# Kernel tuning notes

Measured on AMD Instinct MI355X. Metric: run time of the kernel, lower is better.

## Reference

```python
import jax, jax.numpy as jnp
import numpy as np

BN, SN = 16, 64
C, T, FY, FX = 480, 8, 28, 28
OS = 8            # roialign output_size
NDF = 256
K = 64            # n_clusters
ALPHA = 1.0
IMG_W, IMG_H = 1920.0, 1080.0
SPATIAL_SCALE = 1.0


def _roi_align(feat, boxes):
    """torchvision RoIAlign with sampling_ratio=1, aligned=True.
    feat: [bn, C, H, W]; boxes: [bn, sn, 4] (x1,y1,x2,y2) in feature coords.
    Returns [bn, sn, C, OS, OS]."""
    bn, c, H, W = feat.shape
    xy1 = boxes[..., 0:2] * SPATIAL_SCALE - 0.5   # aligned=True offset
    xy2 = boxes[..., 2:4] * SPATIAL_SCALE - 0.5
    bin_wh = (xy2 - xy1) / OS                     # [bn,sn,2]
    ctr = jnp.arange(OS, dtype=feat.dtype) + 0.5  # one sample per bin (ratio=1)
    xs = xy1[..., 0:1] + ctr * bin_wh[..., 0:1]   # [bn,sn,OS]
    ys = xy1[..., 1:2] + ctr * bin_wh[..., 1:2]
    X = xs[:, :, None, :]                         # [bn,sn,1,OS]
    Y = ys[:, :, :, None]                         # [bn,sn,OS,1]
    valid = (Y > -1.0) & (Y < H) & (X > -1.0) & (X < W)
    x = jnp.clip(X, 0.0, W - 1.0)
    y = jnp.clip(Y, 0.0, H - 1.0)
    x0 = jnp.floor(x).astype(jnp.int32)
    y0 = jnp.floor(y).astype(jnp.int32)
    x1 = jnp.minimum(x0 + 1, W - 1)
    y1 = jnp.minimum(y0 + 1, H - 1)
    lx = x - x0
    ly = y - y0
    fhw = jnp.transpose(feat, (0, 2, 3, 1))       # [bn,H,W,C]
    g = jax.vmap(lambda f, yy, xx: f[yy, xx])     # broadcasting gather -> [bn,sn,OS,OS,C]
    v00 = g(fhw, y0, x0); v01 = g(fhw, y0, x1)
    v10 = g(fhw, y1, x0); v11 = g(fhw, y1, x1)
    wy0, wy1 = (1.0 - ly)[..., None], ly[..., None]
    wx0, wx1 = (1.0 - lx)[..., None], lx[..., None]
    out = v00 * wy0 * wx0 + v01 * wy0 * wx1 + v10 * wy1 * wx0 + v11 * wy1 * wx1
    out = jnp.where(valid[..., None], out, 0.0)
    return jnp.transpose(out, (0, 1, 4, 2, 3))    # [bn,sn,C,OS,OS] (torch layout)


def setup_inputs() -> dict:
    key = jax.random.key(0)
    ks = jax.random.split(key, 6)
    z_vis = jax.random.normal(ks[0], (BN, C, T, FY, FX), jnp.float32)
    # valid boxes (x1<x2, y1<y2), fully inside the image -> no NaN padding rows
    tl = jax.random.uniform(ks[1], (BN, SN, 2)) * jnp.array([IMG_W * 0.5, IMG_H * 0.5])
    wh = jax.random.uniform(ks[2], (BN, SN, 2)) * jnp.array([IMG_W * 0.4, IMG_H * 0.4]) + 16.0
    bboxs = jnp.concatenate([tl, tl + wh], axis=-1).astype(jnp.float32)
    W_vis = jax.random.normal(ks[3], (C * OS * OS, NDF), jnp.float32) / np.sqrt(C * OS * OS)
    b_vis = jnp.zeros((NDF,), jnp.float32)
    W_spc = jax.random.normal(ks[4], (1, NDF), jnp.float32)
    b_spc = jnp.zeros((NDF,), jnp.float32)
    centroids = jax.random.normal(ks[5], (K, NDF), jnp.float32) * 0.1
    return {"z_vis": z_vis, "bboxs": bboxs, "W_vis": W_vis, "b_vis": b_vis,
            "W_spc": W_spc, "b_spc": b_spc, "centroids": centroids}


def reference(z_vis, bboxs, W_vis, b_vis, W_spc, b_spc, centroids):
    bn, sn = bboxs.shape[:2]
    # scale image-coord boxes to feature-map coords
    scale = jnp.array([FX / IMG_W, FY / IMG_H], dtype=z_vis.dtype)
    boxes_f = (bboxs.reshape(bn, sn, 2, 2) * scale).reshape(bn, sn, 4)
    feat = z_vis[:, :, -1]                                   # last temporal frame [bn,C,fy,fx]
    roi = _roi_align(feat, boxes_f).reshape(bn, sn, -1)      # [bn,sn,C*OS*OS]
    z_v = roi @ W_vis + b_vis                                # visual embedding [bn,sn,NDF]
    # spatial embedding: normalized distance of bbox center to image center (detached)
    b2 = bboxs.reshape(bn, sn, 2, 2)
    ctr = b2[:, :, 0] + (b2[:, :, 1] - b2[:, :, 0]) * 0.5    # [bn,sn,2]
    img_c = jnp.array([IMG_W / 2.0, IMG_H / 2.0], dtype=z_vis.dtype)
    norms = jnp.linalg.norm(ctr - img_c, axis=-1, keepdims=True) / jnp.linalg.norm(img_c)
    norms = jax.lax.stop_gradient(norms)                     # .detach() in original
    z_s = norms @ W_spc + b_spc                              # [bn,sn,NDF]
    z = z_v + z_s
    # Student-t soft assignment on L2 distance (NOT squared, as in the source)
    d = jnp.linalg.norm(z[:, :, None, :] - centroids, axis=-1)   # [bn,sn,K]
    s_un = (1.0 + d / ALPHA) ** (-(ALPHA + 1.0) / 2.0)
    s = s_un / jnp.sum(s_un, axis=-1, keepdims=True)
    c = jnp.argmax(s, axis=-1)
    return z, s, c
```

## Files before the change

kernel.cpp:

```cpp
#include <hip/hip_runtime.h>
#include <cstdint>
#include <cstddef>

#define BN_   16
#define C_    480
#define T_    8
#define FY_   28
#define FX_   28
#define NDF_  256
#define KC_   64
#define M_    1024
#define KD_   30720
#define PLANE_ 784
#define CHSTRIDE_ (T_*PLANE_)
#define CT_   (C_*CHSTRIDE_)
#define KS_   32
#define KCH_  960
#define NCH_  15
#define NSTEP_ 30
#define MT_   32
#define APAD_ 72
#define BTILE_ 16384

typedef __attribute__((ext_vector_type(8))) short bf16x8;
typedef __attribute__((ext_vector_type(4))) float f32x4;

__device__ __forceinline__ unsigned rne_bf16(float f) {
    union { float f; unsigned u; } v; v.f = f;
    return v.u + 0x7FFFu + ((v.u >> 16) & 1u);
}
__device__ __forceinline__ float bfbits_to_f(unsigned r) {
    union { unsigned u; float f; } v; v.u = r & 0xFFFF0000u;
    return v.f;
}

__global__ __launch_bounds__(256)
void convert_pack(const float* __restrict__ W, unsigned short* __restrict__ Bpack) {
    const int blk = blockIdx.x;
    const int kb = blk * 32;
    const int n = threadIdx.x;
    unsigned hw[16], lw[16];
    #pragma unroll
    for (int p = 0; p < 16; ++p) {
        const float v0 = W[(size_t)(kb + 2 * p) * NDF_ + n];
        const float v1 = W[(size_t)(kb + 2 * p + 1) * NDF_ + n];
        const unsigned h0 = rne_bf16(v0), h1 = rne_bf16(v1);
        const unsigned l0 = rne_bf16(v0 - bfbits_to_f(h0));
        const unsigned l1 = rne_bf16(v1 - bfbits_to_f(h1));
        hw[p] = __builtin_amdgcn_perm(h1, h0, 0x07060302u);
        lw[p] = __builtin_amdgcn_perm(l1, l0, 0x07060302u);
    }
    unsigned short* hb = Bpack + (size_t)blk * BTILE_;
    unsigned short* lb = hb + 8192;
    uint4* ho = (uint4*)hb + n * 4;
    uint4* lo = (uint4*)lb + n * 4;
    #pragma unroll
    for (int q = 0; q < 4; ++q) {
        ho[q] = make_uint4(hw[q * 4 + 0], hw[q * 4 + 1], hw[q * 4 + 2], hw[q * 4 + 3]);
        lo[q] = make_uint4(lw[q * 4 + 0], lw[q * 4 + 1], lw[q * 4 + 2], lw[q * 4 + 3]);
    }
}

__global__ void convert_cent(const float* __restrict__ cent, float* __restrict__ centT) {
    const int k = blockIdx.x;
    const int j = threadIdx.x;
    centT[(size_t)j * KC_ + k] = cent[(size_t)k * NDF_ + j];
}

__global__ __launch_bounds__(256, 3)
void gemm_fused(const float* __restrict__ z_vis, const unsigned short* __restrict__ Bpack,
                const float* __restrict__ bboxs, float* __restrict__ z_acc) {
    __shared__ short Ah[MT_ * APAD_];
    __shared__ short Al[MT_ * APAD_];
    __shared__ unsigned short Bh[256 * 32];
    __shared__ unsigned short Bl[256 * 32];
    __shared__ float Pl[PLANE_];

    const int t = threadIdx.x;
    const int ks = blockIdx.x, mi = blockIdx.y;
    const int lane = t & 63, wid = t >> 6;

    const int m = t >> 3, by = t & 7;
    const int roi = mi * MT_ + m;
    const int bn = mi >> 1;

    int xi0[8], xi1[8];
    float xw0[8], xw1[8];
    int yr0, yr1;
    float wy0v, wy1v;
    {
        const float bx1 = bboxs[roi * 4 + 0], by1 = bboxs[roi * 4 + 1];
        const float bx2 = bboxs[roi * 4 + 2], by2 = bboxs[roi * 4 + 3];
        const float sx = 28.0f / 1920.0f, sy = 28.0f / 1080.0f;
        const float lo_x = bx1 * sx - 0.5f;
        const float binw_x = (bx2 * sx - 0.5f - lo_x) * 0.125f;
        const float lo_y = by1 * sy - 0.5f;
        const float binw_y = (by2 * sy - 0.5f - lo_y) * 0.125f;
        #pragma unroll
        for (int b = 0; b < 8; ++b) {
            const float pos = lo_x + ((float)b + 0.5f) * binw_x;
            const float vx = (pos > -1.0f && pos < 28.0f) ? 1.0f : 0.0f;
            const float pc = fminf(fmaxf(pos, 0.0f), 27.0f);
            const float p0 = floorf(pc);
            const float lx = pc - p0;
            xi0[b] = (int)p0;
            xi1[b] = min(xi0[b] + 1, 27);
            xw0[b] = vx * (1.0f - lx);
            xw1[b] = vx * lx;
        }
        const float pos = lo_y + ((float)by + 0.5f) * binw_y;
        const float vy = (pos > -1.0f && pos < 28.0f) ? 1.0f : 0.0f;
        const float pc = fminf(fmaxf(pos, 0.0f), 27.0f);
        const float p0 = floorf(pc);
        const float ly = pc - p0;
        const int y0 = (int)p0, y1 = min(y0 + 1, 27);
        yr0 = y0 * FX_; yr1 = y1 * FX_;
        wy0v = vy * (1.0f - ly); wy1v = vy * ly;
    }
    const float* plane = z_vis + (size_t)bn * CT_ + (size_t)(T_ - 1) * PLANE_;

    auto plane_load = [&](int cc) {
        if (wid != 0) return;
        const char* gb = (const char*)(plane + (size_t)(ks * NCH_ + cc) * CHSTRIDE_);
        #pragma unroll
        for (int i = 0; i < 3; ++i)
            __builtin_amdgcn_global_load_lds(
                (const __attribute__((address_space(1))) void*)(gb + (i * 64 + lane) * 16),
                (__attribute__((address_space(3))) void*)((char*)Pl + i * 1024), 16, 0, 0);
        if (lane < 4)
            __builtin_amdgcn_global_load_lds(
                (const __attribute__((address_space(1))) void*)(gb + (192 + lane) * 16),
                (__attribute__((address_space(3))) void*)((char*)Pl + 3072), 16, 0, 0);
    };

    auto stage_B = [&](int s) {
        const unsigned short* hb = Bpack + (size_t)(ks * NSTEP_ + s) * BTILE_;
        #pragma unroll
        for (int qq = 0; qq < 4; ++qq) {
            const int off = (qq * 64 + wid * 16) * 32;
            __builtin_amdgcn_global_load_lds(
                (const __attribute__((address_space(1))) void*)(hb + off + lane * 8),
                (__attribute__((address_space(3))) void*)&Bh[off], 16, 0, 0);
            __builtin_amdgcn_global_load_lds(
                (const __attribute__((address_space(1))) void*)(hb + 8192 + off + lane * 8),
                (__attribute__((address_space(3))) void*)&Bl[off], 16, 0, 0);
        }
    };

    auto stage_A = [&]() {
        unsigned rh[8], rl[8];
        #pragma unroll
        for (int b = 0; b < 8; ++b) {
            const float v00 = Pl[yr0 + xi0[b]], v01 = Pl[yr0 + xi1[b]];
            const float v10 = Pl[yr1 + xi0[b]], v11 = Pl[yr1 + xi1[b]];
            const float val = wy0v * (xw0[b] * v00 + xw1[b] * v01)
                            + wy1v * (xw0[b] * v10 + xw1[b] * v11);
            rh[b] = rne_bf16(val);
            rl[b] = rne_bf16(val - bfbits_to_f(rh[b]));
        }
        const uint4 hh = make_uint4(__builtin_amdgcn_perm(rh[1], rh[0], 0x07060302u),
                                    __builtin_amdgcn_perm(rh[3], rh[2], 0x07060302u),
                                    __builtin_amdgcn_perm(rh[5], rh[4], 0x07060302u),
                                    __builtin_amdgcn_perm(rh[7], rh[6], 0x07060302u));
        const uint4 ll = make_uint4(__builtin_amdgcn_perm(rl[1], rl[0], 0x07060302u),
                                    __builtin_amdgcn_perm(rl[3], rl[2], 0x07060302u),
                                    __builtin_amdgcn_perm(rl[5], rl[4], 0x07060302u),
                                    __builtin_amdgcn_perm(rl[7], rl[6], 0x07060302u));
        *(uint4*)&Ah[m * APAD_ + by * 8] = hh;
        *(uint4*)&Al[m * APAD_ + by * 8] = ll;
    };

    const int fr = lane & 15, fq = lane >> 4;
    f32x4 acc[2][4] = {};

    plane_load(0);
    stage_B(0);
    __syncthreads();
    stage_A();

    for (int cc = 0; cc < NCH_; ++cc) {
        #pragma unroll
        for (int half = 0; half < 2; ++half) {
            const int s = 2 * cc + half;
            __syncthreads();

            bf16x8 afh[2], afl[2], bh[4], bl[4];
            #pragma unroll
            for (int i = 0; i < 2; ++i) {
                afh[i] = *(const bf16x8*)&Ah[(i * 16 + fr) * APAD_ + half * 32 + fq * 8];
                afl[i] = *(const bf16x8*)&Al[(i * 16 + fr) * APAD_ + half * 32 + fq * 8];
            }
            #pragma unroll
            for (int j = 0; j < 4; ++j) {
                bh[j] = *(const bf16x8*)&Bh[(wid * 64 + j * 16 + fr) * 32 + fq * 8];
                bl[j] = *(const bf16x8*)&Bl[(wid * 64 + j * 16 + fr) * 32 + fq * 8];
            }
            __syncthreads();

            if (half == 0) {
                stage_B(s + 1);
                if (cc + 1 < NCH_) plane_load(cc + 1);
            } else if (cc + 1 < NCH_) {
                stage_B(s + 1);
                stage_A();
            }

            #pragma unroll
            for (int j = 0; j < 4; ++j)
                #pragma unroll
                for (int i = 0; i < 2; ++i) {
                    acc[i][j] = __builtin_amdgcn_mfma_f32_16x16x32_bf16(afh[i], bh[j], acc[i][j], 0, 0, 0);
                    acc[i][j] = __builtin_amdgcn_mfma_f32_16x16x32_bf16(afl[i], bh[j], acc[i][j], 0, 0, 0);
                    acc[i][j] = __builtin_amdgcn_mfma_f32_16x16x32_bf16(afh[i], bl[j], acc[i][j], 0, 0, 0);
                }
        }
    }

    #pragma unroll
    for (int i = 0; i < 2; ++i) {
        const int row = mi * MT_ + i * 16 + fq * 4;
        #pragma unroll
        for (int j = 0; j < 4; ++j) {
            const int col = wid * 64 + j * 16 + fr;
            #pragma unroll
            for (int r = 0; r < 4; ++r)
                atomicAdd(&z_acc[(size_t)(row + r) * NDF_ + col], acc[i][j][r]);
        }
    }
}

__global__ __launch_bounds__(256)
void cluster_kernel(const float* __restrict__ z_acc, const float* __restrict__ bboxs,
                    const float* __restrict__ b_vis, const float* __restrict__ W_spc,
                    const float* __restrict__ b_spc, const float* __restrict__ centT,
                    float* __restrict__ out) {
    const int row = blockIdx.x, t = threadIdx.x;
    __shared__ float zs[NDF_];
    __shared__ float dp[4][KC_];

    const float a = z_acc[(size_t)row * NDF_ + t];

    const float x1 = bboxs[row * 4 + 0], y1 = bboxs[row * 4 + 1];
    const float x2 = bboxs[row * 4 + 2], y2 = bboxs[row * 4 + 3];
    const float cx = x1 + (x2 - x1) * 0.5f - 960.0f;
    const float cy = y1 + (y2 - y1) * 0.5f - 540.0f;
    const float nrm = sqrtf(cx * cx + cy * cy) / sqrtf(960.0f * 960.0f + 540.0f * 540.0f);

    const float zj = a + b_vis[t] + nrm * W_spc[t] + b_spc[t];
    zs[t] = zj;
    out[(size_t)row * NDF_ + t] = zj;
    __syncthreads();

    const int k = t & 63, qq = t >> 6;
    {
        float d2 = 0.0f;
        const float* ct = centT + (size_t)qq * 64 * KC_;
        #pragma unroll 8
        for (int j = 0; j < 64; ++j) {
            const float df = zs[qq * 64 + j] - ct[(size_t)j * KC_ + k];
            d2 += df * df;
        }
        dp[qq][k] = d2;
    }
    __syncthreads();

    if (t < 64) {
        const float d = sqrtf(dp[0][t] + dp[1][t] + dp[2][t] + dp[3][t]);
        const float su = 1.0f / (1.0f + d);
        float sum = su;
        #pragma unroll
        for (int mk = 1; mk < 64; mk <<= 1) sum += __shfl_xor(sum, mk, 64);
        out[(size_t)M_ * NDF_ + (size_t)row * KC_ + t] = su / sum;
        float v = d; int idx = t;
        #pragma unroll
        for (int mk = 1; mk < 64; mk <<= 1) {
            const float ov = __shfl_xor(v, mk, 64);
            const int oi = __shfl_xor(idx, mk, 64);
            if (ov < v || (ov == v && oi < idx)) { v = ov; idx = oi; }
        }
        if (t == 0)
            out[(size_t)M_ * NDF_ + (size_t)M_ * KC_ + row] = (float)idx;
    }
}

extern "C" void kernel_launch(void* const* d_in, const int* in_sizes, int n_in,
                              void* d_out, int out_size, void* d_ws, size_t ws_size,
                              hipStream_t stream) {
    const float* z_vis = (const float*)d_in[0];
    const float* bboxs = (const float*)d_in[1];
    const float* W_vis = (const float*)d_in[2];
    const float* b_vis = (const float*)d_in[3];
    const float* W_spc = (const float*)d_in[4];
    const float* b_spc = (const float*)d_in[5];
    const float* cent  = (const float*)d_in[6];
    float* out = (float*)d_out;

    char* ws = (char*)d_ws;
    unsigned short* Bpack = (unsigned short*)ws;
    float*          centT = (float*)(ws + 31457280);
    float*          z_acc = (float*)(ws + 31457280 + 65536);

    convert_pack<<<KS_ * NSTEP_, 256, 0, stream>>>(W_vis, Bpack);
    convert_cent<<<KC_, 256, 0, stream>>>(cent, centT);
    hipMemsetAsync(z_acc, 0, (size_t)M_ * NDF_ * sizeof(float), stream);
    gemm_fused<<<dim3(KS_, M_ / MT_), 256, 0, stream>>>(z_vis, Bpack, bboxs, z_acc);
    cluster_kernel<<<M_, 256, 0, stream>>>(z_acc, bboxs, b_vis, W_spc, b_spc, centT, out);
}
```

Before: 370.4 us.

## Double M tile to one batch per block and restage LDS layouts conflict-free

Result: faster. 346.9 us (-6.3%).

```diff
diff --git a/kernel.cpp b/kernel.cpp
--- a/kernel.cpp
+++ b/kernel.cpp
@@ -18,8 +18,8 @@
 #define KCH_  960
 #define NCH_  15
 #define NSTEP_ 30
-#define MT_   32
-#define APAD_ 72
+#define MT_   64
+#define AOS_  520
 #define BTILE_ 16384
 
 typedef __attribute__((ext_vector_type(8))) short bf16x8;
@@ -32,6 +32,10 @@
 __device__ __forceinline__ float bfbits_to_f(unsigned r) {
     union { unsigned u; float f; } v; v.u = r & 0xFFFF0000u;
     return v.f;
+}
+__device__ __forceinline__ void lds_dma16(const void* g, void* l) {
+    __builtin_amdgcn_global_load_lds((const __attribute__((address_space(1))) void*)g,
+                                     (__attribute__((address_space(3))) void*)l, 16, 0, 0);
 }
 
 __global__ __launch_bounds__(256)
@@ -50,14 +54,12 @@
         hw[p] = __builtin_amdgcn_perm(h1, h0, 0x07060302u);
         lw[p] = __builtin_amdgcn_perm(l1, l0, 0x07060302u);
     }
-    unsigned short* hb = Bpack + (size_t)blk * BTILE_;
-    unsigned short* lb = hb + 8192;
-    uint4* ho = (uint4*)hb + n * 4;
-    uint4* lo = (uint4*)lb + n * 4;
+    uint4* hb4 = (uint4*)(Bpack + (size_t)blk * BTILE_);
+    uint4* lb4 = hb4 + 1024;
     #pragma unroll
-    for (int q = 0; q < 4; ++q) {
-        ho[q] = make_uint4(hw[q * 4 + 0], hw[q * 4 + 1], hw[q * 4 + 2], hw[q * 4 + 3]);
-        lo[q] = make_uint4(lw[q * 4 + 0], lw[q * 4 + 1], lw[q * 4 + 2], lw[q * 4 + 3]);
+    for (int o = 0; o < 4; ++o) {
+        hb4[o * 256 + n] = make_uint4(hw[o * 4 + 0], hw[o * 4 + 1], hw[o * 4 + 2], hw[o * 4 + 3]);
+        lb4[o * 256 + n] = make_uint4(lw[o * 4 + 0], lw[o * 4 + 1], lw[o * 4 + 2], lw[o * 4 + 3]);
     }
 }
 
@@ -67,27 +69,26 @@
     centT[(size_t)j * KC_ + k] = cent[(size_t)k * NDF_ + j];
 }
 
-__global__ __launch_bounds__(256, 3)
+__global__ __launch_bounds__(256, 2)
 void gemm_fused(const float* __restrict__ z_vis, const unsigned short* __restrict__ Bpack,
                 const float* __restrict__ bboxs, float* __restrict__ z_acc) {
-    __shared__ short Ah[MT_ * APAD_];
-    __shared__ short Al[MT_ * APAD_];
-    __shared__ unsigned short Bh[256 * 32];
-    __shared__ unsigned short Bl[256 * 32];
+    __shared__ short Ah[8 * AOS_];
+    __shared__ short Al[8 * AOS_];
+    __shared__ unsigned short Bh[8192];
+    __shared__ unsigned short Bl[8192];
     __shared__ float Pl[PLANE_];
 
     const int t = threadIdx.x;
     const int ks = blockIdx.x, mi = blockIdx.y;
     const int lane = t & 63, wid = t >> 6;
 
-    const int m = t >> 3, by = t & 7;
+    const int m = t >> 2, byl = t & 3;
     const int roi = mi * MT_ + m;
-    const int bn = mi >> 1;
 
     int xi0[8], xi1[8];
     float xw0[8], xw1[8];
-    int yr0, yr1;
-    float wy0v, wy1v;
+    int yr0[2], yr1[2];
+    float wy0[2], wy1[2];
     {
         const float bx1 = bboxs[roi * 4 + 0], by1 = bboxs[roi * 4 + 1];
         const float bx2 = bboxs[roi * 4 + 2], by2 = bboxs[roi * 4 + 3];
@@ -108,70 +109,71 @@
             xw0[b] = vx * (1.0f - lx);
             xw1[b] = vx * lx;
         }
-        const float pos = lo_y + ((float)by + 0.5f) * binw_y;
-        const float vy = (pos > -1.0f && pos < 28.0f) ? 1.0f : 0.0f;
-        const float pc = fminf(fmaxf(pos, 0.0f), 27.0f);
-        const float p0 = floorf(pc);
-        const float ly = pc - p0;
-        const int y0 = (int)p0, y1 = min(y0 + 1, 27);
-        yr0 = y0 * FX_; yr1 = y1 * FX_;
-        wy0v = vy * (1.0f - ly); wy1v = vy * ly;
-    }
-    const float* plane = z_vis + (size_t)bn * CT_ + (size_t)(T_ - 1) * PLANE_;
+        #pragma unroll
+        for (int h = 0; h < 2; ++h) {
+            const int by = byl + h * 4;
+            const float pos = lo_y + ((float)by + 0.5f) * binw_y;
+            const float vy = (pos > -1.0f && pos < 28.0f) ? 1.0f : 0.0f;
+            const float pc = fminf(fmaxf(pos, 0.0f), 27.0f);
+            const float p0 = floorf(pc);
+            const float ly = pc - p0;
+            const int y0 = (int)p0, y1 = min(y0 + 1, 27);
+            yr0[h] = y0 * FX_; yr1[h] = y1 * FX_;
+            wy0[h] = vy * (1.0f - ly); wy1[h] = vy * ly;
+        }
+    }
+    const float* plane = z_vis + (size_t)mi * CT_ + (size_t)(T_ - 1) * PLANE_;
 
     auto plane_load = [&](int cc) {
-        if (wid != 0) return;
         const char* gb = (const char*)(plane + (size_t)(ks * NCH_ + cc) * CHSTRIDE_);
-        #pragma unroll
-        for (int i = 0; i < 3; ++i)
-            __builtin_amdgcn_global_load_lds(
-                (const __attribute__((address_space(1))) void*)(gb + (i * 64 + lane) * 16),
-                (__attribute__((address_space(3))) void*)((char*)Pl + i * 1024), 16, 0, 0);
-        if (lane < 4)
-            __builtin_amdgcn_global_load_lds(
-                (const __attribute__((address_space(1))) void*)(gb + (192 + lane) * 16),
-                (__attribute__((address_space(3))) void*)((char*)Pl + 3072), 16, 0, 0);
+        if (wid < 3) {
+            lds_dma16(gb + (wid * 64 + lane) * 16, (char*)Pl + wid * 1024);
+        } else if (lane < 4) {
+            lds_dma16(gb + (192 + lane) * 16, (char*)Pl + 3072);
+        }
     };
 
     auto stage_B = [&](int s) {
-        const unsigned short* hb = Bpack + (size_t)(ks * NSTEP_ + s) * BTILE_;
+        const char* hb = (const char*)(Bpack + (size_t)(ks * NSTEP_ + s) * BTILE_);
         #pragma unroll
         for (int qq = 0; qq < 4; ++qq) {
-            const int off = (qq * 64 + wid * 16) * 32;
-            __builtin_amdgcn_global_load_lds(
-                (const __attribute__((address_space(1))) void*)(hb + off + lane * 8),
-                (__attribute__((address_space(3))) void*)&Bh[off], 16, 0, 0);
-            __builtin_amdgcn_global_load_lds(
-                (const __attribute__((address_space(1))) void*)(hb + 8192 + off + lane * 8),
-                (__attribute__((address_space(3))) void*)&Bl[off], 16, 0, 0);
+            const int chunk = (qq * 4 + wid) * 1024;
+            lds_dma16(hb + chunk + lane * 16, (char*)Bh + chunk);
+            lds_dma16(hb + 16384 + chunk + lane * 16, (char*)Bl + chunk);
         }
     };
 
     auto stage_A = [&]() {
-        unsigned rh[8], rl[8];
-        #pragma unroll
-        for (int b = 0; b < 8; ++b) {
-            const float v00 = Pl[yr0 + xi0[b]], v01 = Pl[yr0 + xi1[b]];
-            const float v10 = Pl[yr1 + xi0[b]], v11 = Pl[yr1 + xi1[b]];
-            const float val = wy0v * (xw0[b] * v00 + xw1[b] * v01)
-                            + wy1v * (xw0[b] * v10 + xw1[b] * v11);
-            rh[b] = rne_bf16(val);
-            rl[b] = rne_bf16(val - bfbits_to_f(rh[b]));
-        }
-        const uint4 hh = make_uint4(__builtin_amdgcn_perm(rh[1], rh[0], 0x07060302u),
-                                    __builtin_amdgcn_perm(rh[3], rh[2], 0x07060302u),
-                                    __builtin_amdgcn_perm(rh[5], rh[4], 0x07060302u),
-                                    __builtin_amdgcn_perm(rh[7], rh[6], 0x07060302u));
-        const uint4 ll = make_uint4(__builtin_amdgcn_perm(rl[1], rl[0], 0x07060302u),
-                                    __builtin_amdgcn_perm(rl[3], rl[2], 0x07060302u),
-                                    __builtin_amdgcn_perm(rl[5], rl[4], 0x07060302u),
-                                    __builtin_amdgcn_perm(rl[7], rl[6], 0x07060302u));
-        *(uint4*)&Ah[m * APAD_ + by * 8] = hh;
-        *(uint4*)&Al[m * APAD_ + by * 8] = ll;
+        #pragma unroll
+        for (int h = 0; h < 2; ++h) {
+            const int by = byl + h * 4;
+            const int r0 = yr0[h], r1 = yr1[h];
+            const float w0 = wy0[h], w1 = wy1[h];
+            unsigned rh[8], rl[8];
+            #pragma unroll
+            for (int b = 0; b < 8; ++b) {
+                const float v00 = Pl[r0 + xi0[b]], v01 = Pl[r0 + xi1[b]];
+                const float v10 = Pl[r1 + xi0[b]], v11 = Pl[r1 + xi1[b]];
+                const float val = w0 * (xw0[b] * v00 + xw1[b] * v01)
+                                + w1 * (xw0[b] * v10 + xw1[b] * v11);
+                rh[b] = rne_bf16(val);
+                rl[b] = rne_bf16(val - bfbits_to_f(rh[b]));
+            }
+            const uint4 hh = make_uint4(__builtin_amdgcn_perm(rh[1], rh[0], 0x07060302u),
+                                        __builtin_amdgcn_perm(rh[3], rh[2], 0x07060302u),
+                                        __builtin_amdgcn_perm(rh[5], rh[4], 0x07060302u),
+                                        __builtin_amdgcn_perm(rh[7], rh[6], 0x07060302u));
+            const uint4 ll = make_uint4(__builtin_amdgcn_perm(rl[1], rl[0], 0x07060302u),
+                                        __builtin_amdgcn_perm(rl[3], rl[2], 0x07060302u),
+                                        __builtin_amdgcn_perm(rl[5], rl[4], 0x07060302u),
+                                        __builtin_amdgcn_perm(rl[7], rl[6], 0x07060302u));
+            *(uint4*)&Ah[by * AOS_ + m * 8] = hh;
+            *(uint4*)&Al[by * AOS_ + m * 8] = ll;
+        }
     };
 
     const int fr = lane & 15, fq = lane >> 4;
-    f32x4 acc[2][4] = {};
+    f32x4 acc[4][4] = {};
 
     plane_load(0);
     stage_B(0);
@@ -184,16 +186,18 @@
             const int s = 2 * cc + half;
             __syncthreads();
 
-            bf16x8 afh[2], afl[2], bh[4], bl[4];
-            #pragma unroll
-            for (int i = 0; i < 2; ++i) {
-                afh[i] = *(const bf16x8*)&Ah[(i * 16 + fr) * APAD_ + half * 32 + fq * 8];
-                afl[i] = *(const bf16x8*)&Al[(i * 16 + fr) * APAD_ + half * 32 + fq * 8];
+            bf16x8 afh[4], afl[4], bh[4], bl[4];
+            #pragma unroll
+            for (int i = 0; i < 4; ++i) {
+                const int ao = (half * 4 + fq) * AOS_ + (i * 16 + fr) * 8;
+                afh[i] = *(const bf16x8*)&Ah[ao];
+                afl[i] = *(const bf16x8*)&Al[ao];
             }
             #pragma unroll
             for (int j = 0; j < 4; ++j) {
-                bh[j] = *(const bf16x8*)&Bh[(wid * 64 + j * 16 + fr) * 32 + fq * 8];
-                bl[j] = *(const bf16x8*)&Bl[(wid * 64 + j * 16 + fr) * 32 + fq * 8];
+                const int bo = fq * 2048 + (wid * 64 + j * 16 + fr) * 8;
+                bh[j] = *(const bf16x8*)&Bh[bo];
+                bl[j] = *(const bf16x8*)&Bl[bo];
             }
             __syncthreads();
 
@@ -208,7 +212,7 @@
             #pragma unroll
             for (int j = 0; j < 4; ++j)
                 #pragma unroll
-                for (int i = 0; i < 2; ++i) {
+                for (int i = 0; i < 4; ++i) {
                     acc[i][j] = __builtin_amdgcn_mfma_f32_16x16x32_bf16(afh[i], bh[j], acc[i][j], 0, 0, 0);
                     acc[i][j] = __builtin_amdgcn_mfma_f32_16x16x32_bf16(afl[i], bh[j], acc[i][j], 0, 0, 0);
                     acc[i][j] = __builtin_amdgcn_mfma_f32_16x16x32_bf16(afh[i], bl[j], acc[i][j], 0, 0, 0);
@@ -217,7 +221,7 @@
     }
 
     #pragma unroll
-    for (int i = 0; i < 2; ++i) {
+    for (int i = 0; i < 4; ++i) {
         const int row = mi * MT_ + i * 16 + fq * 4;
         #pragma unroll
         for (int j = 0; j < 4; ++j) {
```
